# Optimization experiments

Measured on AMD Instinct MI355X. Metric: run time of the kernel, lower is better.

## Reference

```python
import jax, jax.numpy as jnp
import numpy as np

# Pangu-Weather EarthAttention3D, dim=192 branch
H = 6                 # heads
D = 192               # dim
DH = D // H           # head dim = 32
N = 2 * 6 * 12        # window tokens = 144
TW = (8 // 2) * (186 // 6)  # type_of_windows = 124
NW = 8                # number of windows (leading batch axis)
SCALE = DH ** -0.5


def setup_inputs() -> dict:
    key = jax.random.key(0)
    ks = jax.random.split(key, 7)
    return {
        "x": jax.random.normal(ks[0], (NW, TW, N, D), jnp.float32),
        "mask": jax.random.normal(ks[1], (NW, TW, N, N), jnp.float32),
        "w_qkv": jax.random.normal(ks[2], (D, 3 * D), jnp.float32) * 0.02,
        "b_qkv": jnp.zeros((3 * D,), jnp.float32),
        "bias": jax.random.normal(ks[3], (1, TW, H, N, N), jnp.float32) * 0.02,
        "w_out": jax.random.normal(ks[4], (D, D), jnp.float32) * 0.02,
        "b_out": jnp.zeros((D,), jnp.float32),
    }


def reference(x, mask, w_qkv, b_qkv, bias, w_out, b_out):
    B, W, Ntok, Dm = x.shape  # (nW, type_of_windows, win_tokens, dim)
    # fused QKV projection
    qkv = (x @ w_qkv + b_qkv).reshape(B, W, Ntok, 3, H, DH)
    qkv = jnp.transpose(qkv, (3, 0, 1, 4, 2, 5))  # (3, B, W, H, N, dh)
    q, k, v = qkv[0] * SCALE, qkv[1], qkv[2]
    # scores + earth-specific bias + window mask (broadcast over heads)
    attn = jnp.einsum('bwhnd,bwhmd->bwhnm', q, k)
    attn = attn + bias + mask[:, :, None, :, :]
    attn = jax.nn.softmax(attn, axis=-1)  # dropout_rate=0 -> identity
    out = jnp.einsum('bwhnm,bwhmd->bwhnd', attn, v)
    out = jnp.transpose(out, (0, 1, 3, 2, 4)).reshape(B, W, Ntok, Dm)
    return out @ w_out + b_out
```

## Files before the change

kernel.cpp:

```cpp
#include <hip/hip_runtime.h>
#include <hip/hip_bf16.h>

typedef __bf16 bf16_t;
typedef bf16_t bf16x8 __attribute__((ext_vector_type(8)));
typedef bf16_t bf16x4 __attribute__((ext_vector_type(4)));
typedef float f32x4 __attribute__((ext_vector_type(4)));

#define SCALE 0.17677669529663687f

#define PIN(x) asm volatile("" : "+v"(x))

__device__ __forceinline__ int swz_elem(int r, int c) {
    int g = c >> 3;
    return r * 192 + ((g >> 3) << 6) + (((g & 7) ^ (r & 7)) << 3) + (c & 7);
}

__device__ __forceinline__ void stage_chunk(bf16_t* dst, const bf16_t* src, int tid) {
#pragma unroll
    for (int it = 0; it < 3; ++it) {
        int off = (it * 256 + tid) * 8;
        __builtin_amdgcn_global_load_lds(
            (const __attribute__((address_space(1))) unsigned int*)(src + off),
            (__attribute__((address_space(3))) unsigned int*)(dst + off),
            16, 0, 0);
    }
}

__global__ void prep_weights(const float* __restrict__ w_qkv, const float* __restrict__ w_out,
                             bf16_t* __restrict__ wqkvS, bf16_t* __restrict__ woutS) {
    int i = blockIdx.x * 256 + threadIdx.x;
    if (i < 576 * 192) {
        int o = i / 192, k = i % 192;
        float v = w_qkv[k * 576 + o];
        if (o < 192) v *= SCALE;
        wqkvS[(o >> 5) * 6144 + swz_elem(o & 31, k)] = (bf16_t)v;
    }
    if (i < 192 * 192) {
        int o = i / 192, k = i % 192;
        woutS[(o >> 5) * 6144 + swz_elem(o & 31, k)] = (bf16_t)w_out[k * 192 + o];
    }
}

__global__ __launch_bounds__(256)
void prep_bm(const float* __restrict__ bias, const float* __restrict__ mask,
             bf16_t* __restrict__ biasP, bf16_t* __restrict__ maskP)
{
    int gid = blockIdx.x * 256 + threadIdx.x;
    const int NB = 6696 * 64;
    const int NM = 8928 * 64;
    bool isMask = gid >= NB;
    if (isMask) gid -= NB;
    if (isMask && gid >= NM) return;
    const int lane = gid & 63;
    const int region = gid >> 6;
    const int lrow = lane & 15, lgrp = lane >> 4;
    const int t = region % 9, rg = region / 9;
    const float* src = (isMask ? mask : bias) + ((size_t)rg * 144 + t * 16 + lrow) * 144 + lgrp * 4;
    bf16_t* dst = (isMask ? maskP : biasP) + (size_t)region * 2560 + lane * 8;
#pragma unroll
    for (int it = 0; it < 5; ++it) {
        f32x4 v0 = *(const f32x4*)(src + it * 32);
        bf16x8 o;
        o[0] = (bf16_t)v0[0]; o[1] = (bf16_t)v0[1]; o[2] = (bf16_t)v0[2]; o[3] = (bf16_t)v0[3];
        if (it < 4) {
            f32x4 v1 = *(const f32x4*)(src + it * 32 + 16);
            o[4] = (bf16_t)v1[0]; o[5] = (bf16_t)v1[1]; o[6] = (bf16_t)v1[2]; o[7] = (bf16_t)v1[3];
        } else {
            o[4] = o[5] = o[6] = o[7] = (bf16_t)0.f;
        }
        *(bf16x8*)(dst + it * 512) = o;
    }
}

__global__ __launch_bounds__(256, 4)
void qkv_gemm(const float* __restrict__ x, const float* __restrict__ b_qkv,
              const bf16_t* __restrict__ wqkvS,
              bf16_t* __restrict__ Qg, bf16_t* __restrict__ Kg, bf16_t* __restrict__ Vt)
{
    __shared__ __align__(16) bf16_t Wb[2][6144];
    __shared__ __align__(16) bf16_t T[4][1280];
    const int tid  = threadIdx.x;
    const int lane = tid & 63;
    const int wave = tid >> 6;
    const int lrow = lane & 15;
    const int lgrp = lane >> 4;
    const int r0   = blockIdx.x * 128 + wave * 32;

    stage_chunk(&Wb[0][0], wqkvS, tid);

    bf16x8 af[2][6];
#pragma unroll
    for (int tt = 0; tt < 2; ++tt)
#pragma unroll
        for (int ks = 0; ks < 6; ++ks) {
            const float* px = x + (size_t)(r0 + tt * 16 + lrow) * 192 + ks * 32 + lgrp * 8;
            f32x4 lo = *(const f32x4*)px;
            f32x4 hi = *(const f32x4*)(px + 4);
            bf16x8 v;
            v[0] = (bf16_t)lo[0]; v[1] = (bf16_t)lo[1]; v[2] = (bf16_t)lo[2]; v[3] = (bf16_t)lo[3];
            v[4] = (bf16_t)hi[0]; v[5] = (bf16_t)hi[1]; v[6] = (bf16_t)hi[2]; v[7] = (bf16_t)hi[3];
            af[tt][ks] = v;
        }
    __syncthreads();

    bf16_t* tl = &T[wave][0];

    for (int hc = 0; hc < 18; ++hc) {
        if (hc < 17) stage_chunk(&Wb[(hc + 1) & 1][0], wqkvS + (hc + 1) * 6144, tid);
        const bf16_t* wb = &Wb[hc & 1][0];

        f32x4 a[2][2];
        a[0][0] = f32x4{0.f,0.f,0.f,0.f}; a[0][1] = f32x4{0.f,0.f,0.f,0.f};
        a[1][0] = f32x4{0.f,0.f,0.f,0.f}; a[1][1] = f32x4{0.f,0.f,0.f,0.f};
#pragma unroll
        for (int ks = 0; ks < 6; ++ks) {
            bf16x8 wf0 = *(const bf16x8*)&wb[swz_elem(lrow,      ks * 32 + lgrp * 8)];
            bf16x8 wf1 = *(const bf16x8*)&wb[swz_elem(16 + lrow, ks * 32 + lgrp * 8)];
#pragma unroll
            for (int tt = 0; tt < 2; ++tt) {
                a[tt][0] = __builtin_amdgcn_mfma_f32_16x16x32_bf16(af[tt][ks], wf0, a[tt][0], 0, 0, 0);
                a[tt][1] = __builtin_amdgcn_mfma_f32_16x16x32_bf16(af[tt][ks], wf1, a[tt][1], 0, 0, 0);
            }
        }
        __syncthreads();

        float b0 = b_qkv[hc * 32 + lrow], b1 = b_qkv[hc * 32 + 16 + lrow];
        if (hc < 6) { b0 *= SCALE; b1 *= SCALE; }

        if (hc < 12) {
            const int h = (hc < 6) ? hc : hc - 6;
            bf16_t* dst = (hc < 6) ? Qg : Kg;
#pragma unroll
            for (int tt = 0; tt < 2; ++tt) {
#pragma unroll
                for (int j = 0; j < 4; ++j) {
                    tl[tt * 640 + (lgrp * 4 + j) * 40 + lrow]      = (bf16_t)(a[tt][0][j] + b0);
                    tl[tt * 640 + (lgrp * 4 + j) * 40 + 16 + lrow] = (bf16_t)(a[tt][1][j] + b1);
                }
                bf16x8 val = *(const bf16x8*)&tl[tt * 640 + lrow * 40 + lgrp * 8];
                int tk = r0 + tt * 16 + lrow, bw = tk / 144, n = tk % 144;
                *(bf16x8*)&dst[((size_t)(bw * 6 + h) * 144 + n) * 32 + lgrp * 8] = val;
            }
        } else {
            const int hv = hc - 12;
#pragma unroll
            for (int tt = 0; tt < 2; ++tt)
#pragma unroll
                for (int j = 0; j < 4; ++j) {
                    tl[(lrow) * 40      + tt * 16 + lgrp * 4 + j] = (bf16_t)(a[tt][0][j] + b0);
                    tl[(16 + lrow) * 40 + tt * 16 + lgrp * 4 + j] = (bf16_t)(a[tt][1][j] + b1);
                }
#pragma unroll
            for (int it = 0; it < 2; ++it) {
                int slot = it * 64 + lane;
                int d = slot >> 2, c = slot & 3;
                int tk = r0 + c * 8, bw = tk / 144, n = tk % 144;
                bf16x8 val = *(const bf16x8*)&tl[d * 40 + c * 8];
                *(bf16x8*)&Vt[((size_t)(bw * 6 + hv) * 32 + d) * 160 + n] = val;
            }
        }
    }
}

__global__ __launch_bounds__(256, 2)
void earth_attn_v8(const bf16_t* __restrict__ Qg, const bf16_t* __restrict__ Kg,
                   const bf16_t* __restrict__ Vt,
                   const bf16_t* __restrict__ maskP, const bf16_t* __restrict__ biasP,
                   bf16_t* __restrict__ Og)
{
    __shared__ bf16_t P[4][16 * 168];
    const int tid  = threadIdx.x;
    const int lane = tid & 63;
    const int wave = tid >> 6;
    const int lrow = lane & 15;
    const int lgrp = lane >> 4;

    const int orig = blockIdx.x;
    const int blk  = (orig & 7) * 186 + (orig >> 3);

    const int wid = blk * 4 + wave;
    const int ww  = wid / 48;
    const int r1  = wid % 48;
    const int b   = r1 / 6;
    const int h   = r1 % 6;
    const int bw  = b * 124 + ww;

    const size_t kbase = ((size_t)(bw * 6 + h) * 144) * 32;
    const size_t vbase = ((size_t)(bw * 6 + h) * 32) * 160;

    bf16x8 ka[9];
#pragma unroll
    for (int nt = 0; nt < 9; ++nt)
        ka[nt] = *(const bf16x8*)&Kg[kbase + (size_t)(nt * 16 + lrow) * 32 + lgrp * 8];

    bf16x8 va0[5], va1[5];
#pragma unroll
    for (int ks = 0; ks < 5; ++ks) {
        va0[ks] = *(const bf16x8*)&Vt[vbase + (size_t)lrow * 160 + ks * 32 + lgrp * 8];
        va1[ks] = *(const bf16x8*)&Vt[vbase + (size_t)(16 + lrow) * 160 + ks * 32 + lgrp * 8];
    }

    const bf16_t* bpB = biasP + (size_t)(ww * 6 + h) * 9 * 2560 + lane * 8;
    const bf16_t* mpB = maskP + (size_t)bw * 9 * 2560 + lane * 8;
    bf16_t* pb = &P[wave][0];
    bf16_t* ogp = Og + ((size_t)bw * 144) * 192 + h * 32 + lgrp * 8;

    bf16x8 qa = *(const bf16x8*)&Qg[kbase + (size_t)lrow * 32 + lgrp * 8];
    bf16x8 bvv[5], mvv[5];
#pragma unroll
    for (int it = 0; it < 5; ++it) {
        bvv[it] = *(const bf16x8*)(bpB + it * 512);
        mvv[it] = *(const bf16x8*)(mpB + it * 512);
    }

#pragma unroll 1
    for (int t = 0; t < 9; ++t) {
        f32x4 s[9];
#pragma unroll
        for (int nt = 0; nt < 9; ++nt)
#pragma unroll
            for (int j = 0; j < 4; ++j) {
                const int u = nt * 4 + j;
                s[nt][j] = (float)bvv[u >> 3][u & 7] + (float)mvv[u >> 3][u & 7];
            }

        const int tn = (t < 8) ? t + 1 : 8;
        bf16x8 qa_n = *(const bf16x8*)&Qg[kbase + (size_t)(tn * 16 + lrow) * 32 + lgrp * 8];
        PIN(qa_n);
#pragma unroll
        for (int it = 0; it < 5; ++it) {
            bvv[it] = *(const bf16x8*)(bpB + (size_t)tn * 2560 + it * 512);
            mvv[it] = *(const bf16x8*)(mpB + (size_t)tn * 2560 + it * 512);
        }
#pragma unroll
        for (int it = 0; it < 5; ++it) { PIN(bvv[it]); PIN(mvv[it]); }

#pragma unroll
        for (int nt = 0; nt < 9; ++nt)
            s[nt] = __builtin_amdgcn_mfma_f32_16x16x32_bf16(ka[nt], qa, s[nt], 0, 0, 0);

        float mx = -1e30f;
#pragma unroll
        for (int nt = 0; nt < 9; ++nt)
#pragma unroll
            for (int j = 0; j < 4; ++j) mx = fmaxf(mx, s[nt][j]);
        mx = fmaxf(mx, __shfl_xor(mx, 16, 64));
        mx = fmaxf(mx, __shfl_xor(mx, 32, 64));
        float sum = 0.f;
#pragma unroll
        for (int nt = 0; nt < 9; ++nt)
#pragma unroll
            for (int j = 0; j < 4; ++j) { float e = __expf(s[nt][j] - mx); s[nt][j] = e; sum += e; }
        sum += __shfl_xor(sum, 16, 64);
        sum += __shfl_xor(sum, 32, 64);
        const float rinv = 1.0f / sum;

#pragma unroll
        for (int nt = 0; nt < 9; ++nt) {
            bf16x4 pw;
#pragma unroll
            for (int j = 0; j < 4; ++j) pw[j] = (bf16_t)(s[nt][j] * rinv);
            *(bf16x4*)&pb[lrow * 168 + nt * 16 + lgrp * 4] = pw;
        }
        {
            uint2 z2 = make_uint2(0u, 0u);
            *(uint2*)&pb[lrow * 168 + 144 + lgrp * 4] = z2;
        }

        bf16x8 pa[5];
#pragma unroll
        for (int ks = 0; ks < 5; ++ks)
            pa[ks] = *(const bf16x8*)&pb[lrow * 168 + ks * 32 + lgrp * 8];
#pragma unroll
        for (int ks = 0; ks < 5; ++ks) PIN(pa[ks]);

        f32x4 o0{0.f, 0.f, 0.f, 0.f}, o1{0.f, 0.f, 0.f, 0.f};
#pragma unroll
        for (int ks = 0; ks < 5; ++ks) {
            o0 = __builtin_amdgcn_mfma_f32_16x16x32_bf16(pa[ks], va0[ks], o0, 0, 0, 0);
            o1 = __builtin_amdgcn_mfma_f32_16x16x32_bf16(pa[ks], va1[ks], o1, 0, 0, 0);
        }

#pragma unroll
        for (int j = 0; j < 4; ++j) {
            pb[(lgrp * 4 + j) * 168 + lrow]      = (bf16_t)o0[j];
            pb[(lgrp * 4 + j) * 168 + 16 + lrow] = (bf16_t)o1[j];
        }
        bf16x8 ov = *(const bf16x8*)&pb[lrow * 168 + lgrp * 8];
        *(bf16x8*)(ogp + (size_t)(t * 16 + lrow) * 192) = ov;

        qa = qa_n;
    }
}

__global__ __launch_bounds__(256, 2)
void earth_attn_v7(const bf16_t* __restrict__ Qg, const bf16_t* __restrict__ Kg,
                   const bf16_t* __restrict__ Vt,
                   const float* __restrict__ mask, const float* __restrict__ bias,
                   bf16_t* __restrict__ Og)
{
    __shared__ bf16_t P[4][16 * 168];
    const int tid  = threadIdx.x;
    const int lane = tid & 63;
    const int wave = tid >> 6;
    const int lrow = lane & 15;
    const int lgrp = lane >> 4;
    const int orig = blockIdx.x;
    const int blk  = (orig & 7) * 186 + (orig >> 3);
    const int wid = blk * 4 + wave;
    const int ww  = wid / 48;
    const int r1  = wid % 48;
    const int b   = r1 / 6;
    const int h   = r1 % 6;
    const int bw  = b * 124 + ww;
    const size_t kbase = ((size_t)(bw * 6 + h) * 144) * 32;
    const size_t vbase = ((size_t)(bw * 6 + h) * 32) * 160;

    bf16x8 ka[9];
#pragma unroll
    for (int nt = 0; nt < 9; ++nt)
        ka[nt] = *(const bf16x8*)&Kg[kbase + (size_t)(nt * 16 + lrow) * 32 + lgrp * 8];
    bf16x8 va0[5], va1[5];
#pragma unroll
    for (int ks = 0; ks < 5; ++ks) {
        va0[ks] = *(const bf16x8*)&Vt[vbase + (size_t)lrow * 160 + ks * 32 + lgrp * 8];
        va1[ks] = *(const bf16x8*)&Vt[vbase + (size_t)(16 + lrow) * 160 + ks * 32 + lgrp * 8];
    }
    const float* bp_base = bias + (size_t)(ww * 6 + h) * 144 * 144;
    const float* mp_base = mask + (size_t)bw * 144 * 144;
    bf16_t* pb = &P[wave][0];
    bf16_t* ogp = Og + ((size_t)bw * 144) * 192 + h * 32 + lgrp * 8;
    bf16x8 qa = *(const bf16x8*)&Qg[kbase + (size_t)lrow * 32 + lgrp * 8];
    f32x4 bv[9], mv[9];
    {
        const float* bp = bp_base + (size_t)lrow * 144;
        const float* mp = mp_base + (size_t)lrow * 144;
#pragma unroll
        for (int nt = 0; nt < 9; ++nt) {
            bv[nt] = *(const f32x4*)(bp + nt * 16 + lgrp * 4);
            mv[nt] = *(const f32x4*)(mp + nt * 16 + lgrp * 4);
        }
    }
#pragma unroll 1
    for (int t = 0; t < 9; ++t) {
        f32x4 s[9];
#pragma unroll
        for (int nt = 0; nt < 9; ++nt) s[nt] = bv[nt] + mv[nt];
        const int tn = (t < 8) ? t + 1 : 8;
        bf16x8 qa_n = *(const bf16x8*)&Qg[kbase + (size_t)(tn * 16 + lrow) * 32 + lgrp * 8];
        PIN(qa_n);
        {
            const float* bp = bp_base + (size_t)(tn * 16 + lrow) * 144;
            const float* mp = mp_base + (size_t)(tn * 16 + lrow) * 144;
#pragma unroll
            for (int nt = 0; nt < 9; ++nt) {
                bv[nt] = *(const f32x4*)(bp + nt * 16 + lgrp * 4);
                mv[nt] = *(const f32x4*)(mp + nt * 16 + lgrp * 4);
            }
#pragma unroll
            for (int nt = 0; nt < 9; ++nt) { PIN(bv[nt]); PIN(mv[nt]); }
        }
#pragma unroll
        for (int nt = 0; nt < 9; ++nt)
            s[nt] = __builtin_amdgcn_mfma_f32_16x16x32_bf16(ka[nt], qa, s[nt], 0, 0, 0);
        float mx = -1e30f;
#pragma unroll
        for (int nt = 0; nt < 9; ++nt)
#pragma unroll
            for (int j = 0; j < 4; ++j) mx = fmaxf(mx, s[nt][j]);
        mx = fmaxf(mx, __shfl_xor(mx, 16, 64));
        mx = fmaxf(mx, __shfl_xor(mx, 32, 64));
        float sum = 0.f;
#pragma unroll
        for (int nt = 0; nt < 9; ++nt)
#pragma unroll
            for (int j = 0; j < 4; ++j) { float e = __expf(s[nt][j] - mx); s[nt][j] = e; sum += e; }
        sum += __shfl_xor(sum, 16, 64);
        sum += __shfl_xor(sum, 32, 64);
        const float rinv = 1.0f / sum;
#pragma unroll
        for (int nt = 0; nt < 9; ++nt) {
            bf16x4 pw;
#pragma unroll
            for (int j = 0; j < 4; ++j) pw[j] = (bf16_t)(s[nt][j] * rinv);
            *(bf16x4*)&pb[lrow * 168 + nt * 16 + lgrp * 4] = pw;
        }
        {
            uint2 z2 = make_uint2(0u, 0u);
            *(uint2*)&pb[lrow * 168 + 144 + lgrp * 4] = z2;
        }
        bf16x8 pa[5];
#pragma unroll
        for (int ks = 0; ks < 5; ++ks)
            pa[ks] = *(const bf16x8*)&pb[lrow * 168 + ks * 32 + lgrp * 8];
#pragma unroll
        for (int ks = 0; ks < 5; ++ks) PIN(pa[ks]);
        f32x4 o0{0.f, 0.f, 0.f, 0.f}, o1{0.f, 0.f, 0.f, 0.f};
#pragma unroll
        for (int ks = 0; ks < 5; ++ks) {
            o0 = __builtin_amdgcn_mfma_f32_16x16x32_bf16(pa[ks], va0[ks], o0, 0, 0, 0);
            o1 = __builtin_amdgcn_mfma_f32_16x16x32_bf16(pa[ks], va1[ks], o1, 0, 0, 0);
        }
#pragma unroll
        for (int j = 0; j < 4; ++j) {
            pb[(lgrp * 4 + j) * 168 + lrow]      = (bf16_t)o0[j];
            pb[(lgrp * 4 + j) * 168 + 16 + lrow] = (bf16_t)o1[j];
        }
        bf16x8 ov = *(const bf16x8*)&pb[lrow * 168 + lgrp * 8];
        *(bf16x8*)(ogp + (size_t)(t * 16 + lrow) * 192) = ov;
        qa = qa_n;
    }
}

__global__ __launch_bounds__(256, 4)
void out_proj(const bf16_t* __restrict__ Og, const bf16_t* __restrict__ woutS,
              const float* __restrict__ b_out, float* __restrict__ out)
{
    __shared__ __align__(16) bf16_t Wb[2][6144];
    const int tid  = threadIdx.x;
    const int lane = tid & 63;
    const int wave = tid >> 6;
    const int lrow = lane & 15;
    const int lgrp = lane >> 4;
    const size_t row0 = (size_t)blockIdx.x * 64 + wave * 16;

    stage_chunk(&Wb[0][0], woutS, tid);

    bf16x8 af[6];
#pragma unroll
    for (int ks = 0; ks < 6; ++ks)
        af[ks] = *(const bf16x8*)(Og + (row0 + lrow) * 192 + ks * 32 + lgrp * 8);
    __syncthreads();

#pragma unroll
    for (int c = 0; c < 6; ++c) {
        if (c < 5) stage_chunk(&Wb[(c + 1) & 1][0], woutS + (c + 1) * 6144, tid);
        const bf16_t* wb = &Wb[c & 1][0];
        float b0 = b_out[c * 32 + lrow], b1 = b_out[c * 32 + 16 + lrow];
        f32x4 a0{b0, b0, b0, b0}, a1{b1, b1, b1, b1};
#pragma unroll
        for (int ks = 0; ks < 6; ++ks) {
            bf16x8 wf0 = *(const bf16x8*)&wb[swz_elem(lrow,      ks * 32 + lgrp * 8)];
            bf16x8 wf1 = *(const bf16x8*)&wb[swz_elem(16 + lrow, ks * 32 + lgrp * 8)];
            a0 = __builtin_amdgcn_mfma_f32_16x16x32_bf16(af[ks], wf0, a0, 0, 0, 0);
            a1 = __builtin_amdgcn_mfma_f32_16x16x32_bf16(af[ks], wf1, a1, 0, 0, 0);
        }
        __syncthreads();
#pragma unroll
        for (int j = 0; j < 4; ++j) {
            out[(row0 + lgrp * 4 + j) * 192 + c * 32 + lrow]      = a0[j];
            out[(row0 + lgrp * 4 + j) * 192 + c * 32 + 16 + lrow] = a1[j];
        }
    }
}

extern "C" void kernel_launch(void* const* d_in, const int* in_sizes, int n_in,
                              void* d_out, int out_size, void* d_ws, size_t ws_size,
                              hipStream_t stream) {
    const float* x     = (const float*)d_in[0];
    const float* mask  = (const float*)d_in[1];
    const float* w_qkv = (const float*)d_in[2];
    const float* b_qkv = (const float*)d_in[3];
    const float* bias  = (const float*)d_in[4];
    const float* w_out = (const float*)d_in[5];
    const float* b_out = (const float*)d_in[6];

    bf16_t* wqkvS = (bf16_t*)d_ws;
    bf16_t* woutS = wqkvS + 576 * 192;
    bf16_t* Qg    = woutS + 192 * 192;
    bf16_t* Kg    = Qg + (size_t)992 * 6 * 144 * 32;
    bf16_t* Vt    = Kg + (size_t)992 * 6 * 144 * 32;
    bf16_t* Og    = Vt + (size_t)992 * 6 * 32 * 160;
    bf16_t* biasP = Og + (size_t)992 * 144 * 192;
    bf16_t* maskP = biasP + (size_t)6696 * 2560;

    const size_t need_v8 = ((size_t)112902144 + 17141760 + 22855680) * 2;

    prep_weights<<<dim3(432), dim3(256), 0, stream>>>(w_qkv, w_out, wqkvS, woutS);
    qkv_gemm<<<dim3(1116), dim3(256), 0, stream>>>(x, b_qkv, wqkvS, Qg, Kg, Vt);

    if (ws_size >= need_v8) {
        prep_bm<<<dim3(3906), dim3(256), 0, stream>>>(bias, mask, biasP, maskP);
        earth_attn_v8<<<dim3(1488), dim3(256), 0, stream>>>(Qg, Kg, Vt, maskP, biasP, Og);
    } else {
        earth_attn_v7<<<dim3(1488), dim3(256), 0, stream>>>(Qg, Kg, Vt, mask, bias, Og);
    }
    out_proj<<<dim3(2232), dim3(256), 0, stream>>>(Og, woutS, b_out, (float*)d_out);
}
```

Before: 285.1 us.

## Split attention per head across three waves with K/V staged in LDS

The attention kernel now assigns one (window, head) pair to a 192-thread block whose three waves each process three of the nine query tiles. K and V are staged once into LDS via global_load_lds and read from there instead of being held in registers per wave. The bias/mask prep kernel now does coalesced row loads into LDS before permuting into the MFMA fragment layout. This aims to raise parallelism, lower register pressure and improve prep coalescing, at the cost of more blocks, LDS traffic and the loss of the previous software prefetch of the next tile's bias and mask.

```diff
diff --git a/kernel.cpp b/kernel.cpp
--- a/kernel.cpp
+++ b/kernel.cpp
@@ -24,6 +24,13 @@
             (__attribute__((address_space(3))) unsigned int*)(dst + off),
             16, 0, 0);
     }
+}
+
+__device__ __forceinline__ void stage_1k(bf16_t* dst, const bf16_t* src, int lane) {
+    __builtin_amdgcn_global_load_lds(
+        (const __attribute__((address_space(1))) unsigned int*)(src + lane * 8),
+        (__attribute__((address_space(3))) unsigned int*)(dst + lane * 8),
+        16, 0, 0);
 }
 
 __global__ void prep_weights(const float* __restrict__ w_qkv, const float* __restrict__ w_out,
@@ -41,34 +48,41 @@
     }
 }
 
-__global__ __launch_bounds__(256)
-void prep_bm(const float* __restrict__ bias, const float* __restrict__ mask,
-             bf16_t* __restrict__ biasP, bf16_t* __restrict__ maskP)
+__global__ __launch_bounds__(256, 8)
+void prep_bm2(const float* __restrict__ bias, const float* __restrict__ mask,
+              bf16_t* __restrict__ biasP, bf16_t* __restrict__ maskP)
 {
-    int gid = blockIdx.x * 256 + threadIdx.x;
-    const int NB = 6696 * 64;
-    const int NM = 8928 * 64;
-    bool isMask = gid >= NB;
-    if (isMask) gid -= NB;
-    if (isMask && gid >= NM) return;
-    const int lane = gid & 63;
-    const int region = gid >> 6;
-    const int lrow = lane & 15, lgrp = lane >> 4;
-    const int t = region % 9, rg = region / 9;
-    const float* src = (isMask ? mask : bias) + ((size_t)rg * 144 + t * 16 + lrow) * 144 + lgrp * 4;
-    bf16_t* dst = (isMask ? maskP : biasP) + (size_t)region * 2560 + lane * 8;
-#pragma unroll
-    for (int it = 0; it < 5; ++it) {
-        f32x4 v0 = *(const f32x4*)(src + it * 32);
+    __shared__ bf16_t L[16 * 148];
+    int blk = blockIdx.x;
+    bool isMask = blk >= 6696;
+    int region = isMask ? blk - 6696 : blk;
+    int rg = region / 9, t = region % 9;
+    const float* src = (isMask ? mask : bias) + ((size_t)rg * 144 + t * 16) * 144;
+    bf16_t* dst = (isMask ? maskP : biasP) + (size_t)region * 2560;
+    const int tid = threadIdx.x;
+
+    for (int i = tid; i < 576; i += 256) {
+        int row = i / 36, seg = i % 36;
+        f32x4 v = *(const f32x4*)(src + row * 144 + seg * 4);
+        bf16x4 o;
+        o[0] = (bf16_t)v[0]; o[1] = (bf16_t)v[1]; o[2] = (bf16_t)v[2]; o[3] = (bf16_t)v[3];
+        *(bf16x4*)&L[row * 148 + seg * 4] = o;
+    }
+    __syncthreads();
+
+    for (int u = tid; u < 320; u += 256) {
+        int it = u >> 6, lane = u & 63;
+        int lrow = lane & 15, lgrp = lane >> 4;
         bf16x8 o;
-        o[0] = (bf16_t)v0[0]; o[1] = (bf16_t)v0[1]; o[2] = (bf16_t)v0[2]; o[3] = (bf16_t)v0[3];
-        if (it < 4) {
-            f32x4 v1 = *(const f32x4*)(src + it * 32 + 16);
-            o[4] = (bf16_t)v1[0]; o[5] = (bf16_t)v1[1]; o[6] = (bf16_t)v1[2]; o[7] = (bf16_t)v1[3];
-        } else {
-            o[4] = o[5] = o[6] = o[7] = (bf16_t)0.f;
-        }
-        *(bf16x8*)(dst + it * 512) = o;
+#pragma unroll
+        for (int e = 0; e < 8; ++e) {
+            int us = it * 8 + e;
+            int nt = us >> 2, j = us & 3;
+            int m = (us < 36) ? (nt * 16 + lgrp * 4 + j) : 0;
+            bf16_t v = L[lrow * 148 + m];
+            o[e] = (us < 36) ? v : (bf16_t)0.f;
+        }
+        *(bf16x8*)(dst + it * 512 + lane * 8) = o;
     }
 }
 
@@ -162,13 +176,15 @@
     }
 }
 
-__global__ __launch_bounds__(256, 2)
-void earth_attn_v8(const bf16_t* __restrict__ Qg, const bf16_t* __restrict__ Kg,
-                   const bf16_t* __restrict__ Vt,
-                   const bf16_t* __restrict__ maskP, const bf16_t* __restrict__ biasP,
-                   bf16_t* __restrict__ Og)
+__global__ __launch_bounds__(192, 3)
+void earth_attn_v10(const bf16_t* __restrict__ Qg, const bf16_t* __restrict__ Kg,
+                    const bf16_t* __restrict__ Vt,
+                    const bf16_t* __restrict__ maskP, const bf16_t* __restrict__ biasP,
+                    bf16_t* __restrict__ Og)
 {
-    __shared__ bf16_t P[4][16 * 168];
+    __shared__ __align__(16) bf16_t Kl[4608];
+    __shared__ __align__(16) bf16_t Vl[5120];
+    __shared__ __align__(16) bf16_t P[3][16 * 168];
     const int tid  = threadIdx.x;
     const int lane = tid & 63;
     const int wave = tid >> 6;
@@ -176,45 +192,43 @@
     const int lgrp = lane >> 4;
 
     const int orig = blockIdx.x;
-    const int blk  = (orig & 7) * 186 + (orig >> 3);
-
-    const int wid = blk * 4 + wave;
-    const int ww  = wid / 48;
-    const int r1  = wid % 48;
-    const int b   = r1 / 6;
-    const int h   = r1 % 6;
-    const int bw  = b * 124 + ww;
+    const int blk  = (orig & 7) * 744 + (orig >> 3);
+
+    const int ww = blk / 48;
+    const int r1 = blk % 48;
+    const int b  = r1 / 6;
+    const int h  = r1 % 6;
+    const int bw = b * 124 + ww;
 
     const size_t kbase = ((size_t)(bw * 6 + h) * 144) * 32;
     const size_t vbase = ((size_t)(bw * 6 + h) * 32) * 160;
 
-    bf16x8 ka[9];
-#pragma unroll
-    for (int nt = 0; nt < 9; ++nt)
-        ka[nt] = *(const bf16x8*)&Kg[kbase + (size_t)(nt * 16 + lrow) * 32 + lgrp * 8];
-
-    bf16x8 va0[5], va1[5];
-#pragma unroll
-    for (int ks = 0; ks < 5; ++ks) {
-        va0[ks] = *(const bf16x8*)&Vt[vbase + (size_t)lrow * 160 + ks * 32 + lgrp * 8];
-        va1[ks] = *(const bf16x8*)&Vt[vbase + (size_t)(16 + lrow) * 160 + ks * 32 + lgrp * 8];
-    }
+    for (int c = wave; c < 9; c += 3)  stage_1k(Kl + c * 512, Kg + kbase + c * 512, lane);
+    for (int c = wave; c < 10; c += 3) stage_1k(Vl + c * 512, Vt + vbase + c * 512, lane);
+
+    bf16_t* pb = &P[wave][0];
+    {
+        uint2 z2 = make_uint2(0u, 0u);
+        *(uint2*)&pb[lrow * 168 + 144 + lgrp * 4] = z2;
+    }
+    __syncthreads();
 
     const bf16_t* bpB = biasP + (size_t)(ww * 6 + h) * 9 * 2560 + lane * 8;
     const bf16_t* mpB = maskP + (size_t)bw * 9 * 2560 + lane * 8;
-    bf16_t* pb = &P[wave][0];
     bf16_t* ogp = Og + ((size_t)bw * 144) * 192 + h * 32 + lgrp * 8;
 
-    bf16x8 qa = *(const bf16x8*)&Qg[kbase + (size_t)lrow * 32 + lgrp * 8];
-    bf16x8 bvv[5], mvv[5];
-#pragma unroll
-    for (int it = 0; it < 5; ++it) {
-        bvv[it] = *(const bf16x8*)(bpB + it * 512);
-        mvv[it] = *(const bf16x8*)(mpB + it * 512);
-    }
-
 #pragma unroll 1
-    for (int t = 0; t < 9; ++t) {
+    for (int i = 0; i < 3; ++i) {
+        const int t = wave + i * 3;
+
+        bf16x8 bvv[5], mvv[5];
+#pragma unroll
+        for (int it = 0; it < 5; ++it) {
+            bvv[it] = *(const bf16x8*)(bpB + (size_t)t * 2560 + it * 512);
+            mvv[it] = *(const bf16x8*)(mpB + (size_t)t * 2560 + it * 512);
+        }
+        bf16x8 qa = *(const bf16x8*)&Qg[kbase + (size_t)(t * 16 + lrow) * 32 + lgrp * 8];
+
         f32x4 s[9];
 #pragma unroll
         for (int nt = 0; nt < 9; ++nt)
@@ -224,20 +238,11 @@
                 s[nt][j] = (float)bvv[u >> 3][u & 7] + (float)mvv[u >> 3][u & 7];
             }
 
-        const int tn = (t < 8) ? t + 1 : 8;
-        bf16x8 qa_n = *(const bf16x8*)&Qg[kbase + (size_t)(tn * 16 + lrow) * 32 + lgrp * 8];
-        PIN(qa_n);
-#pragma unroll
-        for (int it = 0; it < 5; ++it) {
-            bvv[it] = *(const bf16x8*)(bpB + (size_t)tn * 2560 + it * 512);
-            mvv[it] = *(const bf16x8*)(mpB + (size_t)tn * 2560 + it * 512);
-        }
-#pragma unroll
-        for (int it = 0; it < 5; ++it) { PIN(bvv[it]); PIN(mvv[it]); }
-
-#pragma unroll
-        for (int nt = 0; nt < 9; ++nt)
-            s[nt] = __builtin_amdgcn_mfma_f32_16x16x32_bf16(ka[nt], qa, s[nt], 0, 0, 0);
+#pragma unroll
+        for (int nt = 0; nt < 9; ++nt) {
+            bf16x8 ka = *(const bf16x8*)&Kl[(nt * 16 + lrow) * 32 + lgrp * 8];
+            s[nt] = __builtin_amdgcn_mfma_f32_16x16x32_bf16(ka, qa, s[nt], 0, 0, 0);
+        }
 
         float mx = -1e30f;
 #pragma unroll
@@ -262,23 +267,15 @@
             for (int j = 0; j < 4; ++j) pw[j] = (bf16_t)(s[nt][j] * rinv);
             *(bf16x4*)&pb[lrow * 168 + nt * 16 + lgrp * 4] = pw;
         }
-        {
-            uint2 z2 = make_uint2(0u, 0u);
-            *(uint2*)&pb[lrow * 168 + 144 + lgrp * 4] = z2;
-        }
-
-        bf16x8 pa[5];
-#pragma unroll
-        for (int ks = 0; ks < 5; ++ks)
-            pa[ks] = *(const bf16x8*)&pb[lrow * 168 + ks * 32 + lgrp * 8];
-#pragma unroll
-        for (int ks = 0; ks < 5; ++ks) PIN(pa[ks]);
 
         f32x4 o0{0.f, 0.f, 0.f, 0.f}, o1{0.f, 0.f, 0.f, 0.f};
 #pragma unroll
         for (int ks = 0; ks < 5; ++ks) {
-            o0 = __builtin_amdgcn_mfma_f32_16x16x32_bf16(pa[ks], va0[ks], o0, 0, 0, 0);
-            o1 = __builtin_amdgcn_mfma_f32_16x16x32_bf16(pa[ks], va1[ks], o1, 0, 0, 0);
+            bf16x8 pa = *(const bf16x8*)&pb[lrow * 168 + ks * 32 + lgrp * 8];
+            bf16x8 v0 = *(const bf16x8*)&Vl[lrow * 160 + ks * 32 + lgrp * 8];
+            bf16x8 v1 = *(const bf16x8*)&Vl[(16 + lrow) * 160 + ks * 32 + lgrp * 8];
+            o0 = __builtin_amdgcn_mfma_f32_16x16x32_bf16(pa, v0, o0, 0, 0, 0);
+            o1 = __builtin_amdgcn_mfma_f32_16x16x32_bf16(pa, v1, o1, 0, 0, 0);
         }
 
 #pragma unroll
@@ -288,8 +285,6 @@
         }
         bf16x8 ov = *(const bf16x8*)&pb[lrow * 168 + lgrp * 8];
         *(bf16x8*)(ogp + (size_t)(t * 16 + lrow) * 192) = ov;
-
-        qa = qa_n;
     }
 }
 
@@ -348,7 +343,6 @@
         for (int nt = 0; nt < 9; ++nt) s[nt] = bv[nt] + mv[nt];
         const int tn = (t < 8) ? t + 1 : 8;
         bf16x8 qa_n = *(const bf16x8*)&Qg[kbase + (size_t)(tn * 16 + lrow) * 32 + lgrp * 8];
-        PIN(qa_n);
         {
             const float* bp = bp_base + (size_t)(tn * 16 + lrow) * 144;
             const float* mp = mp_base + (size_t)(tn * 16 + lrow) * 144;
@@ -357,8 +351,6 @@
                 bv[nt] = *(const f32x4*)(bp + nt * 16 + lgrp * 4);
                 mv[nt] = *(const f32x4*)(mp + nt * 16 + lgrp * 4);
             }
-#pragma unroll
-            for (int nt = 0; nt < 9; ++nt) { PIN(bv[nt]); PIN(mv[nt]); }
         }
 #pragma unroll
         for (int nt = 0; nt < 9; ++nt)
@@ -474,14 +466,14 @@
     bf16_t* biasP = Og + (size_t)992 * 144 * 192;
     bf16_t* maskP = biasP + (size_t)6696 * 2560;
 
-    const size_t need_v8 = ((size_t)112902144 + 17141760 + 22855680) * 2;
+    const size_t need_v10 = ((size_t)112902144 + 17141760 + 22855680) * 2;
 
     prep_weights<<<dim3(432), dim3(256), 0, stream>>>(w_qkv, w_out, wqkvS, woutS);
     qkv_gemm<<<dim3(1116), dim3(256), 0, stream>>>(x, b_qkv, wqkvS, Qg, Kg, Vt);
 
-    if (ws_size >= need_v8) {
-        prep_bm<<<dim3(3906), dim3(256), 0, stream>>>(bias, mask, biasP, maskP);
-        earth_attn_v8<<<dim3(1488), dim3(256), 0, stream>>>(Qg, Kg, Vt, maskP, biasP, Og);
+    if (ws_size >= need_v10) {
+        prep_bm2<<<dim3(15624), dim3(256), 0, stream>>>(bias, mask, biasP, maskP);
+        earth_attn_v10<<<dim3(5952), dim3(192), 0, stream>>>(Qg, Kg, Vt, maskP, biasP, Og);
     } else {
         earth_attn_v7<<<dim3(1488), dim3(256), 0, stream>>>(Qg, Kg, Vt, mask, bias, Og);
     }
```

New measurement: 266.1 us. -6.7%, faster.
